# Kernel optimization log

Hardware: AMD Instinct MI355X
Metric: run time of the kernel (lower is better)

## Reference

```python
import jax, jax.numpy as jnp
import numpy as np

B, T, L, M = 64, 2000, 400, 80
SIGMA_FACTOR = 0.05
SIGMA_CAP = 10.0
SIGMA_MIN = 1.5
WARMUP_STEPS = 10000
GLOBAL_STEP = 0  # fresh loss module -> progress = 0
ENTROPY_TARGET = 3.5
ATTN_W_START = 1.0
ATTN_W_MIN = 0.2
EPS = 1e-8


def setup_inputs() -> dict:
    key = jax.random.key(0)
    ks = jax.random.split(key, 8)
    mel_out_postnet = jax.random.normal(ks[0], (B, T, M), jnp.float32)
    mel_out = jax.random.normal(ks[1], (B, T, M), jnp.float32)
    gate_out = jax.random.normal(ks[2], (B, T), jnp.float32)
    # alignments: stacked per-step attention, row-normalized like real softmax outputs
    a = jax.random.uniform(ks[3], (B, T, L), jnp.float32)
    alignments = a / jnp.sum(a, axis=-1, keepdims=True)
    mel_target = jax.random.normal(ks[4], (B, T, M), jnp.float32)
    gate_target = jnp.round(jax.random.uniform(ks[5], (B, T), jnp.float32))
    mel_lengths = jax.random.randint(ks[6], (B,), T // 2, T + 1, jnp.int32).at[0].set(T)
    text_lengths = jax.random.randint(ks[7], (B,), L // 2, L + 1, jnp.int32).at[0].set(L)
    return {
        "mel_out_postnet": mel_out_postnet, "mel_out": mel_out, "gate_out": gate_out,
        "alignments": alignments, "mel_target": mel_target, "gate_target": gate_target,
        "mel_lengths": mel_lengths, "text_lengths": text_lengths,
    }


def _diagonal_target(text_lengths):
    # sigma per batch element; global_step=0 -> progress=0 -> sigma = init_sigma
    init_sigma = jnp.clip(text_lengths.astype(jnp.float32) * SIGMA_FACTOR, 3.0, SIGMA_CAP)
    progress = min(1.0, GLOBAL_STEP / float(WARMUP_STEPS))
    sigma = init_sigma - (init_sigma - SIGMA_MIN) * progress  # [B]
    t = jnp.arange(T, dtype=jnp.int32)  # decoder steps
    Lb = text_lengths[:, None]  # [B,1]
    # expected_pos = min(int(t*Lb/T), Lb-1); positive ints -> integer floor div matches trunc
    exp_pos = jnp.minimum((t[None, :] * Lb) // T, Lb - 1).astype(jnp.float32)  # [B,T]
    pos = jnp.arange(L, dtype=jnp.float32)  # [L]
    z = (pos[None, None, :] - exp_pos[:, :, None]) / sigma[:, None, None]
    g = jnp.exp(-0.5 * z * z)  # [B,T,L]
    valid = (pos[None, None, :] < text_lengths[:, None, None].astype(jnp.float32))
    g = g * valid
    return g / (jnp.sum(g, axis=-1, keepdims=True) + EPS)


def reference(mel_out_postnet, mel_out, gate_out, alignments, mel_target,
              gate_target, mel_lengths, text_lengths):
    # masked L1 on mel (mel_target already [B,T,M], matching the torch transpose)
    valid = (jnp.arange(T)[None, :] < mel_lengths[:, None])[:, :, None]  # [B,T,1]
    vf = valid.astype(jnp.float32)
    n_valid = jnp.sum(vf) * M
    mel_loss_1 = jnp.sum(jnp.abs(mel_out - mel_target) * vf) / n_valid
    mel_loss_2 = jnp.sum(jnp.abs(mel_out_postnet - mel_target) * vf) / n_valid
    loss_mel = mel_loss_1 + mel_loss_2

    # BCEWithLogits, mean reduction (stable form)
    x, z_t = gate_out, gate_target
    loss_gate = jnp.mean(jnp.maximum(x, 0.0) - x * z_t + jnp.log1p(jnp.exp(-jnp.abs(x))))

    # guided-attention KL against diagonal Gaussian target
    target = _diagonal_target(text_lengths)  # [B,T,L]
    attn_safe = jnp.maximum(alignments, EPS)
    log_pred = jnp.log(attn_safe)
    kl_pw = jnp.where(target > 0.0, target * (jnp.log(jnp.maximum(target, EPS)) - log_pred), 0.0)
    attention_kl = jnp.sum(kl_pw) / B / T  # batchmean then / T_dec
    attention_kl = jnp.minimum(attention_kl, 150.0)

    # entropy-gated attention weight (python-float in torch -> stop_gradient)
    attn_entropy = jnp.mean(-jnp.sum(attn_safe * log_pred, axis=2))
    ratio = jnp.maximum(attn_entropy / ENTROPY_TARGET, 0.0)
    weight = jnp.where(attn_entropy <= ENTROPY_TARGET,
                       jnp.maximum(ATTN_W_MIN, ATTN_W_START * ratio),
                       ATTN_W_START)
    weight = jax.lax.stop_gradient(weight)

    total_loss = loss_mel + loss_gate + weight * attention_kl
    return (total_loss, loss_mel, loss_gate, attention_kl)
```

## Files before the change

kernel.cpp:

```cpp
#include <hip/hip_runtime.h>
#include <cstddef>
#include <cstdint>

#define B_ 64
#define T_ 2000
#define L_ 400
#define M_ 80
#define EPSF 1e-8f
#define LOG_EPSF -18.420680743952367f

#define TBL_N (B_ * L_)
#define NROW (B_ * T_)
#define NBLK 2000

__device__ inline float waveReduce(float v) {
#pragma unroll
  for (int m = 32; m >= 1; m >>= 1) v += __shfl_xor(v, m, 64);
  return v;
}

__global__ __launch_bounds__(256) void table_kernel(
    const int* __restrict__ text_lengths, float4* __restrict__ tbl) {
  const int lane = threadIdx.x & 63;
  const int wid = (blockIdx.x * 256 + threadIdx.x) >> 6;
  if (wid >= TBL_N) return;
  const int b = wid / L_;
  const int epi = wid - b * L_;
  const int Lb = text_lengths[b];
  const float sigma = fminf(fmaxf((float)Lb * 0.05f, 3.0f), 10.0f);
  const float invsig = 1.0f / sigma;
  const float epf = (float)epi;
  float S = 0.f;
#pragma unroll
  for (int k = 0; k < 7; ++k) {
    int l = lane + 64 * k;
    if (l < Lb) {
      float z = ((float)l - epf) * invsig;
      S += __expf(-0.5f * z * z);
    }
  }
  S = waveReduce(S);
  if (lane == 0) {
    float Se = S + EPSF;
    tbl[wid] = make_float4(1.0f / Se, __logf(Se), invsig, 0.f);
  }
}

__global__ __launch_bounds__(256) void expand_kernel(
    const float4* __restrict__ tbl, const int* __restrict__ text_lengths,
    const int* __restrict__ mel_lengths, float4* __restrict__ rowtbl) {
  int p = blockIdx.x * 256 + threadIdx.x;
  if (p >= NROW) return;
  int b = p / T_;
  int t = p - b * T_;
  int Lb = text_lengths[b];
  int epi = t * Lb / T_;
  if (epi > Lb - 1) epi = Lb - 1;
  float4 e = tbl[b * L_ + epi];
  int melv = (t < mel_lengths[b]) ? 1 : 0;
  int w = epi | (Lb << 10) | (melv << 19);
  rowtbl[p] = make_float4(e.x, e.y, e.z, (float)w);
}

__global__ __launch_bounds__(256) void fused_kernel(
    const float4* __restrict__ mo, const float4* __restrict__ mp,
    const float4* __restrict__ mt, const float4* __restrict__ gx,
    const float4* __restrict__ gz, const float4* __restrict__ align4,
    const float4* __restrict__ rowtbl, double* __restrict__ partials) {
  const int tid = threadIdx.x;
  const int base_row = blockIdx.x * 64;
  float mel_acc = 0.f, gate_acc = 0.f, kl_acc = 0.f, ent_acc = 0.f;

  const float4* __restrict__ ab = align4 + (size_t)base_row * (L_ / 4);
  const float4* __restrict__ rt = rowtbl + base_row;
  for (int kk = 0; kk < 5; ++kk) {
    float4 a[5], tb[5];
    int l0[5];
#pragma unroll
    for (int j = 0; j < 5; ++j) {
      int idx = tid + 256 * (kk * 5 + j);
      unsigned r = (unsigned)idx / 100u;
      a[j] = ab[idx];
      tb[j] = rt[r];
      l0[j] = (idx - (int)r * 100) * 4;
    }
#pragma unroll
    for (int j = 0; j < 5; ++j) {
      int wi = (int)tb[j].w;
      float epf = (float)(wi & 1023);
      int Lb = (wi >> 10) & 511;
      float inv = tb[j].x, logSe = tb[j].y, invsig = tb[j].z;
      float av[4] = {a[j].x, a[j].y, a[j].z, a[j].w};
#pragma unroll
      for (int q = 0; q < 4; ++q) {
        float as = fmaxf(av[q], EPSF);
        float lp = __logf(as);
        ent_acc -= as * lp;
        int l = l0[j] + q;
        if (l < Lb) {
          float z = ((float)l - epf) * invsig;
          float e = -0.5f * z * z;
          float tgt = __expf(e) * inv;
          float lt = fmaxf(e - logSe, LOG_EPSF);
          kl_acc += tgt * (lt - lp);
        }
      }
    }
  }

  {
    const float4* __restrict__ mob = mo + (size_t)base_row * (M_ / 4);
    const float4* __restrict__ mpb = mp + (size_t)base_row * (M_ / 4);
    const float4* __restrict__ mtb = mt + (size_t)base_row * (M_ / 4);
    float4 A[5], C[5], D[5];
    int mv[5];
#pragma unroll
    for (int j = 0; j < 5; ++j) {
      int idx = tid + 256 * j;
      unsigned r = (unsigned)idx / 20u;
      A[j] = mob[idx];
      C[j] = mpb[idx];
      D[j] = mtb[idx];
      mv[j] = ((int)rt[r].w) >> 19;
    }
#pragma unroll
    for (int j = 0; j < 5; ++j) {
      if (mv[j]) {
        mel_acc += fabsf(A[j].x - D[j].x) + fabsf(A[j].y - D[j].y)
                 + fabsf(A[j].z - D[j].z) + fabsf(A[j].w - D[j].w)
                 + fabsf(C[j].x - D[j].x) + fabsf(C[j].y - D[j].y)
                 + fabsf(C[j].z - D[j].z) + fabsf(C[j].w - D[j].w);
      }
    }
  }

  if (tid < 16) {
    float4 xv = gx[base_row / 4 + tid];
    float4 zv = gz[base_row / 4 + tid];
    gate_acc = fmaxf(xv.x, 0.f) - xv.x * zv.x + log1pf(__expf(-fabsf(xv.x)))
             + fmaxf(xv.y, 0.f) - xv.y * zv.y + log1pf(__expf(-fabsf(xv.y)))
             + fmaxf(xv.z, 0.f) - xv.z * zv.z + log1pf(__expf(-fabsf(xv.z)))
             + fmaxf(xv.w, 0.f) - xv.w * zv.w + log1pf(__expf(-fabsf(xv.w)));
  }

  float w0 = waveReduce(mel_acc);
  float w1 = waveReduce(gate_acc);
  float w2 = waveReduce(kl_acc);
  float w3 = waveReduce(ent_acc);
  __shared__ double sh[4][4];
  const int lane = threadIdx.x & 63, wib = threadIdx.x >> 6;
  if (lane == 0) {
    sh[wib][0] = (double)w0; sh[wib][1] = (double)w1;
    sh[wib][2] = (double)w2; sh[wib][3] = (double)w3;
  }
  __syncthreads();
  if (tid == 0) {
    partials[blockIdx.x]            = sh[0][0] + sh[1][0] + sh[2][0] + sh[3][0];
    partials[NBLK + blockIdx.x]     = sh[0][1] + sh[1][1] + sh[2][1] + sh[3][1];
    partials[2 * NBLK + blockIdx.x] = sh[0][2] + sh[1][2] + sh[2][2] + sh[3][2];
    partials[3 * NBLK + blockIdx.x] = sh[0][3] + sh[1][3] + sh[2][3] + sh[3][3];
  }
}

__device__ double segSum(const double* __restrict__ p, int n, double* sh) {
  double a = 0.0;
  for (int i = threadIdx.x; i < n; i += 256) a += p[i];
  sh[threadIdx.x] = a;
  __syncthreads();
  for (int s = 128; s > 0; s >>= 1) {
    if ((int)threadIdx.x < s) sh[threadIdx.x] += sh[threadIdx.x + s];
    __syncthreads();
  }
  double r = sh[0];
  __syncthreads();
  return r;
}

__global__ __launch_bounds__(256) void finalize_kernel(
    const double* __restrict__ partials, const int* __restrict__ mel_lengths,
    float* __restrict__ out) {
  __shared__ double sh[256];
  double mel_sum  = segSum(partials, NBLK, sh);
  double gate_sum = segSum(partials + NBLK, NBLK, sh);
  double kl_sum   = segSum(partials + 2 * NBLK, NBLK, sh);
  double ent_sum  = segSum(partials + 3 * NBLK, NBLK, sh);
  if (threadIdx.x == 0) {
    long nv = 0;
    for (int b = 0; b < B_; ++b) nv += mel_lengths[b];
    double n_valid = (double)nv * (double)M_;
    float loss_mel  = (float)(mel_sum / n_valid);
    float loss_gate = (float)(gate_sum / (double)(B_ * T_));
    float kl  = (float)(kl_sum / (double)(B_ * T_));
    kl = fminf(kl, 150.0f);
    float ent = (float)(ent_sum / (double)(B_ * T_));
    float ratio = fmaxf(ent / 3.5f, 0.0f);
    float weight = (ent <= 3.5f) ? fmaxf(0.2f, 1.0f * ratio) : 1.0f;
    out[0] = loss_mel + loss_gate + weight * kl;
    out[1] = loss_mel;
    out[2] = loss_gate;
    out[3] = kl;
  }
}

extern "C" void kernel_launch(void* const* d_in, const int* in_sizes, int n_in,
                              void* d_out, int out_size, void* d_ws, size_t ws_size,
                              hipStream_t stream) {
  const float* mel_out_postnet = (const float*)d_in[0];
  const float* mel_out         = (const float*)d_in[1];
  const float* gate_out        = (const float*)d_in[2];
  const float* alignments      = (const float*)d_in[3];
  const float* mel_target      = (const float*)d_in[4];
  const float* gate_target     = (const float*)d_in[5];
  const int*   mel_lengths     = (const int*)d_in[6];
  const int*   text_lengths    = (const int*)d_in[7];
  float* out = (float*)d_out;

  float4* tbl = (float4*)d_ws;
  float4* rowtbl = (float4*)((char*)d_ws + (size_t)TBL_N * 16);
  double* partials = (double*)((char*)d_ws + (size_t)(TBL_N + NROW) * 16);

  table_kernel<<<dim3((TBL_N * 64 + 255) / 256), dim3(256), 0, stream>>>(
      text_lengths, tbl);
  expand_kernel<<<dim3((NROW + 255) / 256), dim3(256), 0, stream>>>(
      tbl, text_lengths, mel_lengths, rowtbl);
  fused_kernel<<<dim3(NBLK), dim3(256), 0, stream>>>(
      (const float4*)mel_out, (const float4*)mel_out_postnet,
      (const float4*)mel_target, (const float4*)gate_out,
      (const float4*)gate_target, (const float4*)alignments,
      rowtbl, partials);
  finalize_kernel<<<dim3(1), dim3(256), 0, stream>>>(partials, mel_lengths, out);
}
```

Measured before the change: 395.9 us.

## Grid-stride fused loss kernel over more, smaller blocks with sched barriers

Reworks the fused loss kernel so each of 6250 blocks handles 1024 alignment float4s, 512 mel float4s and a grid-strided slice of the gate elements. Previously each of 2000 blocks owned 64 rows. Blocks no longer map to row groups. Sched barriers force all loads to issue before the compute, with the aim of more blocks in flight and more memory-level parallelism. In exchange, the partials array and the finalize reduction grow, and load batching per thread is smaller.

```diff
diff --git a/kernel.cpp b/kernel.cpp
--- a/kernel.cpp
+++ b/kernel.cpp
@@ -11,7 +11,9 @@
 
 #define TBL_N (B_ * L_)
 #define NROW (B_ * T_)
-#define NBLK 2000
+#define NBLK 6250
+#define NA4 (B_ * T_ * (L_ / 4))
+#define NM4 (B_ * T_ * (M_ / 4))
 
 __device__ inline float waveReduce(float v) {
 #pragma unroll
@@ -68,24 +70,22 @@
     const float4* __restrict__ gz, const float4* __restrict__ align4,
     const float4* __restrict__ rowtbl, double* __restrict__ partials) {
   const int tid = threadIdx.x;
-  const int base_row = blockIdx.x * 64;
   float mel_acc = 0.f, gate_acc = 0.f, kl_acc = 0.f, ent_acc = 0.f;
 
-  const float4* __restrict__ ab = align4 + (size_t)base_row * (L_ / 4);
-  const float4* __restrict__ rt = rowtbl + base_row;
-  for (int kk = 0; kk < 5; ++kk) {
-    float4 a[5], tb[5];
-    int l0[5];
-#pragma unroll
-    for (int j = 0; j < 5; ++j) {
-      int idx = tid + 256 * (kk * 5 + j);
+  for (int base = blockIdx.x * 1024; base < NA4; base += NBLK * 1024) {
+    float4 a[4], tb[4];
+    int l0v[4];
+#pragma unroll
+    for (int j = 0; j < 4; ++j) {
+      int idx = base + tid + 256 * j;
       unsigned r = (unsigned)idx / 100u;
-      a[j] = ab[idx];
-      tb[j] = rt[r];
-      l0[j] = (idx - (int)r * 100) * 4;
-    }
-#pragma unroll
-    for (int j = 0; j < 5; ++j) {
+      a[j] = align4[idx];
+      tb[j] = rowtbl[r];
+      l0v[j] = (idx - (int)r * 100) * 4;
+    }
+    __builtin_amdgcn_sched_barrier(0);
+#pragma unroll
+    for (int j = 0; j < 4; ++j) {
       int wi = (int)tb[j].w;
       float epf = (float)(wi & 1023);
       int Lb = (wi >> 10) & 511;
@@ -96,7 +96,7 @@
         float as = fmaxf(av[q], EPSF);
         float lp = __logf(as);
         ent_acc -= as * lp;
-        int l = l0[j] + q;
+        int l = l0v[j] + q;
         if (l < Lb) {
           float z = ((float)l - epf) * invsig;
           float e = -0.5f * z * z;
@@ -108,23 +108,21 @@
     }
   }
 
-  {
-    const float4* __restrict__ mob = mo + (size_t)base_row * (M_ / 4);
-    const float4* __restrict__ mpb = mp + (size_t)base_row * (M_ / 4);
-    const float4* __restrict__ mtb = mt + (size_t)base_row * (M_ / 4);
-    float4 A[5], C[5], D[5];
-    int mv[5];
-#pragma unroll
-    for (int j = 0; j < 5; ++j) {
-      int idx = tid + 256 * j;
+  for (int base = blockIdx.x * 512; base < NM4; base += NBLK * 512) {
+    float4 A[2], C[2], D[2];
+    int mv[2];
+#pragma unroll
+    for (int j = 0; j < 2; ++j) {
+      int idx = base + tid + 256 * j;
       unsigned r = (unsigned)idx / 20u;
-      A[j] = mob[idx];
-      C[j] = mpb[idx];
-      D[j] = mtb[idx];
-      mv[j] = ((int)rt[r].w) >> 19;
-    }
-#pragma unroll
-    for (int j = 0; j < 5; ++j) {
+      A[j] = mo[idx];
+      C[j] = mp[idx];
+      D[j] = mt[idx];
+      mv[j] = ((int)rowtbl[r].w) >> 19;
+    }
+    __builtin_amdgcn_sched_barrier(0);
+#pragma unroll
+    for (int j = 0; j < 2; ++j) {
       if (mv[j]) {
         mel_acc += fabsf(A[j].x - D[j].x) + fabsf(A[j].y - D[j].y)
                  + fabsf(A[j].z - D[j].z) + fabsf(A[j].w - D[j].w)
@@ -134,13 +132,12 @@
     }
   }
 
-  if (tid < 16) {
-    float4 xv = gx[base_row / 4 + tid];
-    float4 zv = gz[base_row / 4 + tid];
-    gate_acc = fmaxf(xv.x, 0.f) - xv.x * zv.x + log1pf(__expf(-fabsf(xv.x)))
-             + fmaxf(xv.y, 0.f) - xv.y * zv.y + log1pf(__expf(-fabsf(xv.y)))
-             + fmaxf(xv.z, 0.f) - xv.z * zv.z + log1pf(__expf(-fabsf(xv.z)))
-             + fmaxf(xv.w, 0.f) - xv.w * zv.w + log1pf(__expf(-fabsf(xv.w)));
+  for (int i = blockIdx.x * 256 + tid; i < (B_ * T_) / 4; i += NBLK * 256) {
+    float4 xv = gx[i], zv = gz[i];
+    gate_acc += fmaxf(xv.x, 0.f) - xv.x * zv.x + log1pf(__expf(-fabsf(xv.x)))
+              + fmaxf(xv.y, 0.f) - xv.y * zv.y + log1pf(__expf(-fabsf(xv.y)))
+              + fmaxf(xv.z, 0.f) - xv.z * zv.z + log1pf(__expf(-fabsf(xv.z)))
+              + fmaxf(xv.w, 0.f) - xv.w * zv.w + log1pf(__expf(-fabsf(xv.w)));
   }
 
   float w0 = waveReduce(mel_acc);
```

New measurement: 405.0 us. 1.02x slower.
